# Optimization experiments

Measured on AMD Instinct MI355X. Metric: run time of the kernel, lower is better.

Reference implementation:

```python
import jax, jax.numpy as jnp
import numpy as np

D_MODEL = 512
N_HEADS = 8
D_HEAD = D_MODEL // N_HEADS
B, S = 4, 2048
NEG_INF = -1e9


def rel_shift(x):
    # x: [B,H,Q,K] -> Transformer-XL relative shift
    b, h, q, k = x.shape
    x = jnp.pad(x, ((0, 0), (0, 0), (0, 0), (1, 0)))  # [B,H,Q,K+1]
    x = x.reshape(b, h, k + 1, q)[:, :, 1:, :]          # drop first row
    return x.reshape(b, h, q, k)


def setup_inputs() -> dict:
    key = jax.random.key(0)
    ks = jax.random.split(key, 9)
    sc = 1.0 / np.sqrt(D_MODEL)
    return {
        "x": jax.random.normal(ks[0], (B, S, D_MODEL), jnp.float32),
        "pos_emb": jax.random.normal(ks[1], (S, D_MODEL), jnp.float32),
        "Wq": jax.random.normal(ks[2], (D_MODEL, D_MODEL), jnp.float32) * sc,
        "Wk": jax.random.normal(ks[3], (D_MODEL, D_MODEL), jnp.float32) * sc,
        "Wv": jax.random.normal(ks[4], (D_MODEL, D_MODEL), jnp.float32) * sc,
        "Wr": jax.random.normal(ks[5], (D_MODEL, D_MODEL), jnp.float32) * sc,
        "Wo": jax.random.normal(ks[6], (D_MODEL, D_MODEL), jnp.float32) * sc,
        "u_bias": jax.random.normal(ks[7], (N_HEADS, D_HEAD), jnp.float32) * 0.02,
        "v_bias": jax.random.normal(ks[8], (N_HEADS, D_HEAD), jnp.float32) * 0.02,
    }


def reference(x, pos_emb, Wq, Wk, Wv, Wr, Wo, u_bias, v_bias):
    b, s, _ = x.shape
    # projections -> [B,S,H,Dh]; relative pos -> [S,H,Dh]
    q = (x @ Wq).reshape(b, s, N_HEADS, D_HEAD)
    k = (x @ Wk).reshape(b, s, N_HEADS, D_HEAD)
    v = (x @ Wv).reshape(b, s, N_HEADS, D_HEAD)
    r = (pos_emb @ Wr).reshape(s, N_HEADS, D_HEAD)

    # content term (AC) and position term (BD, with rel shift)
    ac = jnp.einsum("bihd,bjhd->bhij", q + u_bias, k)
    bd = rel_shift(jnp.einsum("bihd,jhd->bhij", q + v_bias, r))

    scores = (ac + bd) / np.sqrt(D_HEAD)
    causal = jnp.tril(jnp.ones((s, s), bool))
    scores = jnp.where(causal, scores, NEG_INF)
    attn = jax.nn.softmax(scores, axis=-1)  # [B,H,S,S]

    out = jnp.einsum("bhij,bjhd->bihd", attn, v).reshape(b, s, D_MODEL)
    return out @ Wo
```

## Files before the change

### kernel.cpp

```cpp
#include <hip/hip_runtime.h>
#include <math.h>

#define SS 2048
#define BB 4
#define NHD 8
#define BH (BB * NHD)

typedef float f32x4 __attribute__((ext_vector_type(4)));
typedef __bf16 bf16x8 __attribute__((ext_vector_type(8)));

__device__ __forceinline__ short f2bf(float x) {
  unsigned u = __float_as_uint(x);
  unsigned r = (u + 0x7fffu + ((u >> 16) & 1u)) >> 16;
  return (short)r;
}

__device__ __forceinline__ void gld16(const void* g, void* l) {
  __builtin_amdgcn_global_load_lds(
      (const __attribute__((address_space(1))) unsigned int*)g,
      (__attribute__((address_space(3))) unsigned int*)l, 16, 0, 0);
}

__global__ void cast_all(const float* __restrict__ x, const float* __restrict__ pos,
                         short* __restrict__ xb, short* __restrict__ pb, int nx4) {
  int i = blockIdx.x * blockDim.x + threadIdx.x;
  const float4* src;
  short4* dst;
  if (i < nx4) {
    src = (const float4*)x + i;
    dst = (short4*)xb + i;
  } else {
    src = (const float4*)pos + (i - nx4);
    dst = (short4*)pb + (i - nx4);
  }
  float4 v = *src;
  *dst = make_short4(f2bf(v.x), f2bf(v.y), f2bf(v.z), f2bf(v.w));
}

__global__ __launch_bounds__(256) void castT_w(
    const float* __restrict__ W0, const float* __restrict__ W1,
    const float* __restrict__ W2, const float* __restrict__ W3,
    const float* __restrict__ W4, short* __restrict__ T0, short* __restrict__ T1,
    short* __restrict__ T2, short* __restrict__ T3, short* __restrict__ T4) {
  __shared__ float t[64][65];
  const float* W;
  short* T;
  switch (blockIdx.z) {
    case 0: W = W0; T = T0; break;
    case 1: W = W1; T = T1; break;
    case 2: W = W2; T = T2; break;
    case 3: W = W3; T = T3; break;
    default: W = W4; T = T4; break;
  }
  const int k0 = blockIdx.x * 64, n0 = blockIdx.y * 64;
  const int tid = threadIdx.x;
#pragma unroll
  for (int rep = 0; rep < 4; rep++) {
    int idx = rep * 256 + tid;
    int r = idx >> 4, c4 = (idx & 15) << 2;
    float4 v = *(const float4*)&W[(size_t)(k0 + r) * 512 + n0 + c4];
    t[r][c4] = v.x; t[r][c4 + 1] = v.y; t[r][c4 + 2] = v.z; t[r][c4 + 3] = v.w;
  }
  __syncthreads();
#pragma unroll
  for (int rep = 0; rep < 4; rep++) {
    int idx = rep * 256 + tid;
    int n = idx >> 4, k4 = (idx & 15) << 2;
    short4 s = make_short4(f2bf(t[k4][n]), f2bf(t[k4 + 1][n]),
                           f2bf(t[k4 + 2][n]), f2bf(t[k4 + 3][n]));
    *(short4*)&T[(size_t)(n0 + n) * 512 + k0 + k4] = s;
  }
}

__global__ __launch_bounds__(256) void conv_vt(const short* __restrict__ Vh,
                                               short* __restrict__ Vt) {
  __shared__ short t[64][72];
  const int s0 = blockIdx.x * 64, bh = blockIdx.y, tid = threadIdx.x;
#pragma unroll
  for (int rep = 0; rep < 4; rep++) {
    int idx = rep * 256 + tid;
    int r = idx >> 4, c4 = (idx & 15) << 2;
    *(short4*)&t[r][c4] = *(const short4*)&Vh[((size_t)bh * SS + s0 + r) * 64 + c4];
  }
  __syncthreads();
#pragma unroll
  for (int rep = 0; rep < 4; rep++) {
    int idx = rep * 256 + tid;
    int d = idx >> 4, s4 = (idx & 15) << 2;
    short4 o = make_short4(t[s4][d], t[s4 + 1][d], t[s4 + 2][d], t[s4 + 3][d]);
    *(short4*)&Vt[((size_t)bh * 64 + d) * SS + s0 + s4] = o;
  }
}

__device__ __forceinline__ void gemm_core(const short* __restrict__ A,
                                          const short* __restrict__ Bt,
                                          short* lds, int m0, int n0,
                                          f32x4 (&acc)[4][2]) {
  const int tid = threadIdx.x;
  const int lane = tid & 63;
  const int w = tid >> 6;
  const int wr = w >> 2, wc = w & 3;
  const int g = lane >> 4, li = lane & 15;

  auto stage = [&](int buf, int k0) {
#pragma unroll
    for (int i = 0; i < 2; i++) {
      int p = (i * 512 + tid) * 16;
      int qq = p ^ ((p >> 3) & 0x70);
      int row = qq >> 7, col = (qq & 127) >> 1;
      gld16(A + (size_t)(m0 + row) * 512 + k0 + col,
            (char*)(lds + (size_t)buf * 2 * 8192) + p);
      gld16(Bt + (size_t)(n0 + row) * 512 + k0 + col,
            (char*)(lds + ((size_t)buf * 2 + 1) * 8192) + p);
    }
  };

  stage(0, 0);
  __syncthreads();
  int buf = 0;
  for (int t = 0; t < 8; t++) {
    if (t < 7) stage(buf ^ 1, (t + 1) * 64);
    const char* As = (const char*)(lds + (size_t)buf * 2 * 8192);
    const char* Bs = (const char*)(lds + ((size_t)buf * 2 + 1) * 8192);
    bf16x8 af[4][2], bfr[2][2];
#pragma unroll
    for (int ks = 0; ks < 2; ks++) {
      const int cb = g * 16 + ks * 64;
#pragma unroll
      for (int mi = 0; mi < 4; mi++) {
        int row = wr * 64 + mi * 16 + li;
        af[mi][ks] = *(const bf16x8*)(As + row * 128 + (cb ^ ((row & 7) << 4)));
      }
#pragma unroll
      for (int ni = 0; ni < 2; ni++) {
        int row = wc * 32 + ni * 16 + li;
        bfr[ni][ks] = *(const bf16x8*)(Bs + row * 128 + (cb ^ ((row & 7) << 4)));
      }
    }
#pragma unroll
    for (int ks = 0; ks < 2; ks++)
#pragma unroll
      for (int mi = 0; mi < 4; mi++)
#pragma unroll
        for (int ni = 0; ni < 2; ni++)
          acc[mi][ni] = __builtin_amdgcn_mfma_f32_16x16x32_bf16(
              af[mi][ks], bfr[ni][ks], acc[mi][ni], 0, 0, 0);
    __syncthreads();
    buf ^= 1;
  }
}

__global__ __launch_bounds__(512) void proj_gemm(
    const short* __restrict__ A, const short* __restrict__ WtQ,
    const short* __restrict__ WtK, const short* __restrict__ WtV,
    short* __restrict__ Qu, short* __restrict__ Qv, short* __restrict__ Kb,
    short* __restrict__ Vh, const float* __restrict__ ub,
    const float* __restrict__ vb) {
  __shared__ short lds[2][2][128 * 64];
  const int z = blockIdx.z;
  const short* Bt = (z == 0) ? WtQ : (z == 1) ? WtK : WtV;
  const int m0 = blockIdx.x * 128, n0 = blockIdx.y * 128;
  f32x4 acc[4][2] = {};
  gemm_core(A, Bt, &lds[0][0][0], m0, n0, acc);

  const int tid = threadIdx.x;
  const int lane = tid & 63;
  const int w = tid >> 6;
  const int wr = w >> 2, wc = w & 3;
  const int g = lane >> 4, li = lane & 15;
#pragma unroll
  for (int mi = 0; mi < 4; mi++)
#pragma unroll
    for (int ni = 0; ni < 2; ni++) {
      const int n_g = n0 + wc * 32 + ni * 16 + li;
      const int m_b = m0 + wr * 64 + mi * 16 + g * 4;
      const int h = n_g >> 6, d = n_g & 63;
      if (z == 0) {
        const float b0 = ub[n_g], b1 = vb[n_g];
#pragma unroll
        for (int r = 0; r < 4; r++) {
          int m_g = m_b + r;
          size_t ad = ((size_t)((m_g >> 11) * NHD + h) * SS + (m_g & 2047)) * 64 + d;
          Qu[ad] = f2bf(acc[mi][ni][r] + b0);
          Qv[ad] = f2bf(acc[mi][ni][r] + b1);
        }
      } else {
        short* o = (z == 1) ? Kb : Vh;
#pragma unroll
        for (int r = 0; r < 4; r++) {
          int m_g = m_b + r;
          size_t ad = ((size_t)((m_g >> 11) * NHD + h) * SS + (m_g & 2047)) * 64 + d;
          o[ad] = f2bf(acc[mi][ni][r]);
        }
      }
    }
}

template <int EPI>
__global__ __launch_bounds__(512) void mfma_gemm(
    const short* __restrict__ A, const short* __restrict__ Bt,
    short* __restrict__ o0, float* __restrict__ of) {
  __shared__ short lds[2][2][128 * 64];
  const int m0 = blockIdx.x * 128, n0 = blockIdx.y * 128;
  f32x4 acc[4][2] = {};
  gemm_core(A, Bt, &lds[0][0][0], m0, n0, acc);

  const int tid = threadIdx.x;
  const int lane = tid & 63;
  const int w = tid >> 6;
  const int wr = w >> 2, wc = w & 3;
  const int g = lane >> 4, li = lane & 15;
#pragma unroll
  for (int mi = 0; mi < 4; mi++)
#pragma unroll
    for (int ni = 0; ni < 2; ni++) {
      const int n_g = n0 + wc * 32 + ni * 16 + li;
      const int m_b = m0 + wr * 64 + mi * 16 + g * 4;
      if (EPI == 0) {
#pragma unroll
        for (int r = 0; r < 4; r++)
          of[(size_t)(m_b + r) * 512 + n_g] = acc[mi][ni][r];
      } else {
        const int h = n_g >> 6, d = n_g & 63;
#pragma unroll
        for (int r = 0; r < 4; r++) {
          int m_g = m_b + r;
          size_t ad = ((size_t)((m_g >> 11) * NHD + h) * SS + (m_g & 2047)) * 64 + d;
          o0[ad] = f2bf(acc[mi][ni][r]);
        }
      }
    }
}

#define SC2 0.18033688f

__global__ __launch_bounds__(512, 3) void flash_mfma_kernel(
    const short* __restrict__ Qu_, const short* __restrict__ Qv_,
    const short* __restrict__ Kb_, const short* __restrict__ Vt_,
    const short* __restrict__ Rb_, short* __restrict__ AOb) {
  __shared__ __align__(16) unsigned QRl2[8][40 * 25];
  __shared__ __align__(16) short Pl[8][16 * 72];

  const int bx = blockIdx.x;
  const int bh = blockIdx.y;
  const int h = bh & 7;
  const int tid = threadIdx.x;
  const int w = tid >> 6;
  const int wq = w & 3;
  const int qi = (w < 4) ? (31 - bx) : bx;
  const int i0 = qi * 64;
  const int lane = tid & 63;
  const int q = lane & 15;
  const int g = lane >> 4;
  const int dsl = g * 8;

  unsigned* qrw = QRl2[w];
  short* pw = Pl[w];

  const size_t qoff = ((size_t)bh * SS + (i0 + wq * 16 + q)) * 64;
  bf16x8 quF[2], qvF[2];
  quF[0] = *(const bf16x8*)(Qu_ + qoff + dsl);
  quF[1] = *(const bf16x8*)(Qu_ + qoff + dsl + 32);
  qvF[0] = *(const bf16x8*)(Qv_ + qoff + dsl);
  qvF[1] = *(const bf16x8*)(Qv_ + qoff + dsl + 32);

  const int i_my = i0 + wq * 16 + q;

  float m = -1e30f, l = 0.f;
  f32x4 o[4] = {};

  for (int j0 = 0; j0 <= i0; j0 += 64) {
    bf16x8 vf[4][2];
    const size_t vtb = ((size_t)bh * 64) * SS + j0;
#pragma unroll
    for (int ds = 0; ds < 4; ds++)
#pragma unroll
      for (int c = 0; c < 2; c++)
        vf[ds][c] = *(const bf16x8*)(Vt_ + vtb + (size_t)(ds * 16 + q) * SS + dsl + 32 * c);

    f32x4 accS[4] = {};
    f32x4 accR[5] = {};
    const size_t kbase = ((size_t)bh * SS + j0) * 64;
    const int rb0 = SS - 16 + j0 - i0 - 16 * wq;
    const size_t rbase = (size_t)h * SS * 64;
    __builtin_amdgcn_s_setprio(1);
#pragma unroll
    for (int c = 0; c < 2; c++) {
      const int dof = dsl + 32 * c;
#pragma unroll
      for (int ks = 0; ks < 4; ks++) {
        bf16x8 kf = *(const bf16x8*)(Kb_ + kbase + (size_t)(ks * 16 + q) * 64 + dof);
        accS[ks] = __builtin_amdgcn_mfma_f32_16x16x32_bf16(kf, quF[c], accS[ks], 0, 0, 0);
      }
#pragma unroll
      for (int st = 0; st < 5; st++) {
        int rrow = rb0 + st * 16 + q;
        rrow = rrow < SS ? rrow : SS - 1;
        bf16x8 rf = *(const bf16x8*)(Rb_ + rbase + (size_t)rrow * 64 + dof);
        accR[st] = __builtin_amdgcn_mfma_f32_16x16x32_bf16(rf, qvF[c], accR[st], 0, 0, 0);
      }
    }
    __builtin_amdgcn_s_setprio(0);

#pragma unroll
    for (int st = 0; st < 5; st++) {
      unsigned w01 = (unsigned)(unsigned short)f2bf(accR[st][0]) |
                     ((unsigned)(unsigned short)f2bf(accR[st][1]) << 16);
      unsigned w23 = (unsigned)(unsigned short)f2bf(accR[st][2]) |
                     ((unsigned)(unsigned short)f2bf(accR[st][3]) << 16);
      int row = st * 8 + g * 2;
      qrw[row * 25 + q] = w01;
      qrw[(row + 1) * 25 + q] = w23;
    }

    float sreg[4][4];
#pragma unroll
    for (int ks = 0; ks < 4; ks++)
#pragma unroll
      for (int r = 0; r < 4; r++) {
        int krow = ks * 16 + g * 4 + r;
        int t = krow + 15 - q;
        unsigned wv = qrw[(t >> 1) * 25 + q];
        unsigned bits = (t & 1) ? (wv & 0xffff0000u) : (wv << 16);
        float qr = __uint_as_float(bits);
        float sc = (accS[ks][r] + qr) * SC2;
        sreg[ks][r] = (j0 + krow <= i_my) ? sc : -1e30f;
      }

    float b0 = fmaxf(fmaxf(sreg[0][0], sreg[0][1]), fmaxf(sreg[0][2], sreg[0][3]));
    float b1 = fmaxf(fmaxf(sreg[1][0], sreg[1][1]), fmaxf(sreg[1][2], sreg[1][3]));
    float b2 = fmaxf(fmaxf(sreg[2][0], sreg[2][1]), fmaxf(sreg[2][2], sreg[2][3]));
    float b3 = fmaxf(fmaxf(sreg[3][0], sreg[3][1]), fmaxf(sreg[3][2], sreg[3][3]));
    float bmax = fmaxf(fmaxf(b0, b1), fmaxf(b2, b3));
    bmax = fmaxf(bmax, __shfl_xor(bmax, 16, 64));
    bmax = fmaxf(bmax, __shfl_xor(bmax, 32, 64));
    float mnew = fmaxf(m, bmax);
    float scale = __builtin_amdgcn_exp2f(m - mnew);
    float ps[4];
    short4 pk[4];
#pragma unroll
    for (int ks = 0; ks < 4; ks++) {
      float p0 = __builtin_amdgcn_exp2f(sreg[ks][0] - mnew);
      float p1 = __builtin_amdgcn_exp2f(sreg[ks][1] - mnew);
      float p2 = __builtin_amdgcn_exp2f(sreg[ks][2] - mnew);
      float p3 = __builtin_amdgcn_exp2f(sreg[ks][3] - mnew);
      ps[ks] = (p0 + p1) + (p2 + p3);
      pk[ks] = make_short4(f2bf(p0), f2bf(p1), f2bf(p2), f2bf(p3));
    }
    float psum = (ps[0] + ps[1]) + (ps[2] + ps[3]);
    psum += __shfl_xor(psum, 16, 64);
    psum += __shfl_xor(psum, 32, 64);
    l = l * scale + psum;
    m = mnew;

#pragma unroll
    for (int ks = 0; ks < 4; ks++)
      *(short4*)(pw + q * 72 + ks * 16 + g * 4) = pk[ks];

#pragma unroll
    for (int r = 0; r < 4; r++) {
      float sc_r = __shfl(scale, g * 4 + r, 64);
      o[0][r] *= sc_r; o[1][r] *= sc_r; o[2][r] *= sc_r; o[3][r] *= sc_r;
    }

    bf16x8 pf[2];
    pf[0] = *(const bf16x8*)(pw + q * 72 + dsl);
    pf[1] = *(const bf16x8*)(pw + q * 72 + dsl + 32);
    __builtin_amdgcn_s_setprio(1);
#pragma unroll
    for (int ds = 0; ds < 4; ds++)
#pragma unroll
      for (int c = 0; c < 2; c++)
        o[ds] = __builtin_amdgcn_mfma_f32_16x16x32_bf16(pf[c], vf[ds][c], o[ds], 0, 0, 0);
    __builtin_amdgcn_s_setprio(0);
  }

  const int b = bh >> 3;
  float linv = 1.f / l;
#pragma unroll
  for (int r = 0; r < 4; r++) {
    float li2 = __shfl(linv, g * 4 + r, 64);
    int irow = i0 + wq * 16 + g * 4 + r;
    short* op = AOb + ((size_t)(b * SS + irow)) * 512 + h * 64 + q;
#pragma unroll
    for (int ds = 0; ds < 4; ds++) op[ds * 16] = f2bf(o[ds][r] * li2);
  }
}

extern "C" void kernel_launch(void* const* d_in, const int* in_sizes, int n_in,
                              void* d_out, int out_size, void* d_ws,
                              size_t ws_size, hipStream_t stream) {
  const float* x   = (const float*)d_in[0];
  const float* pos = (const float*)d_in[1];
  const float* Wq  = (const float*)d_in[2];
  const float* Wk  = (const float*)d_in[3];
  const float* Wv  = (const float*)d_in[4];
  const float* Wr  = (const float*)d_in[5];
  const float* Wo  = (const float*)d_in[6];
  const float* ub  = (const float*)d_in[7];
  const float* vb  = (const float*)d_in[8];
  float* out = (float*)d_out;

  const size_t BS = (size_t)BB * SS;
  const size_t NX = BS * 512;
  const size_t NR = (size_t)SS * 512;
  const size_t NW = 512 * 512;

  short* xb  = (short*)d_ws;
  short* pb  = xb + NX;
  short* WtQ = pb + NR;
  short* WtK = WtQ + NW;
  short* WtV = WtK + NW;
  short* WtR = WtV + NW;
  short* WtO = WtR + NW;
  short* Qu  = WtO + NW;
  short* Qv  = Qu + NX;
  short* Kb  = Qv + NX;
  short* Vh  = Kb + NX;
  short* Vt  = Vh + NX;
  short* Rb  = Vt + NX;
  short* AOb = Rb + NR;

  cast_all<<<dim3((NX + NR) / 4 / 256), 256, 0, stream>>>(x, pos, xb, pb, (int)(NX / 4));
  castT_w<<<dim3(8, 8, 5), 256, 0, stream>>>(Wq, Wk, Wv, Wr, Wo,
                                             WtQ, WtK, WtV, WtR, WtO);

  proj_gemm<<<dim3(64, 4, 3), 512, 0, stream>>>(xb, WtQ, WtK, WtV,
                                                Qu, Qv, Kb, Vh, ub, vb);
  mfma_gemm<2><<<dim3(16, 4), 512, 0, stream>>>(pb, WtR, Rb, nullptr);
  conv_vt<<<dim3(SS / 64, BH), 256, 0, stream>>>(Vh, Vt);

  flash_mfma_kernel<<<dim3(16, BH), 512, 0, stream>>>(Qu, Qv, Kb, Vt, Rb, AOb);

  mfma_gemm<0><<<dim3(64, 4), 512, 0, stream>>>(AOb, WtO, nullptr, out);
}
```

Measured before the change: 364.0 us.

## Split attention KV range across two blocks and merge partials in combine kernel

The flash-attention kernel moves from paired causal query tiles in 512-thread blocks to 256-thread blocks over a flat grid. Each block processes half of one query tile's key chunks and writes the partial max, sum and unnormalized bf16 output to workspace. A new combine kernel merges the two halves with log-sum-exp rescaling and writes the normalized attention output. This targets better load balance and occupancy, at the cost of an extra launch, extra global traffic, and an added bf16 rounding of the partial outputs. The setprio hints are also removed.

```diff
diff --git a/kernel.cpp b/kernel.cpp
--- a/kernel.cpp
+++ b/kernel.cpp
@@ -8,11 +8,16 @@
 
 typedef float f32x4 __attribute__((ext_vector_type(4)));
 typedef __bf16 bf16x8 __attribute__((ext_vector_type(8)));
+typedef short short8v __attribute__((ext_vector_type(8)));
 
 __device__ __forceinline__ short f2bf(float x) {
   unsigned u = __float_as_uint(x);
   unsigned r = (u + 0x7fffu + ((u >> 16) & 1u)) >> 16;
   return (short)r;
+}
+
+__device__ __forceinline__ float bf2f(short v) {
+  return __uint_as_float(((unsigned)(unsigned short)v) << 16);
 }
 
 __device__ __forceinline__ void gld16(const void* g, void* l) {
@@ -234,28 +239,29 @@
 
 #define SC2 0.18033688f
 
-__global__ __launch_bounds__(512, 3) void flash_mfma_kernel(
+__global__ __launch_bounds__(256, 8) void flash_mfma_kernel(
     const short* __restrict__ Qu_, const short* __restrict__ Qv_,
     const short* __restrict__ Kb_, const short* __restrict__ Vt_,
-    const short* __restrict__ Rb_, short* __restrict__ AOb) {
-  __shared__ __align__(16) unsigned QRl2[8][40 * 25];
-  __shared__ __align__(16) short Pl[8][16 * 72];
-
-  const int bx = blockIdx.x;
-  const int bh = blockIdx.y;
+    const short* __restrict__ Rb_, float* __restrict__ Mp,
+    float* __restrict__ Lp, short* __restrict__ Opb) {
+  __shared__ __align__(16) unsigned QRl[4][40 * 17];
+  __shared__ __align__(16) short Pl[4][16 * 72];
+
+  const int id = blockIdx.x;
+  const int z = id & 1;
+  const int bh = (id >> 1) & 31;
+  const int qi = 31 - (id >> 6);
+  const int i0 = qi * 64;
   const int h = bh & 7;
   const int tid = threadIdx.x;
-  const int w = tid >> 6;
-  const int wq = w & 3;
-  const int qi = (w < 4) ? (31 - bx) : bx;
-  const int i0 = qi * 64;
+  const int wq = tid >> 6;
   const int lane = tid & 63;
   const int q = lane & 15;
   const int g = lane >> 4;
   const int dsl = g * 8;
 
-  unsigned* qrw = QRl2[w];
-  short* pw = Pl[w];
+  unsigned* qrw = QRl[wq];
+  short* pw = Pl[wq];
 
   const size_t qoff = ((size_t)bh * SS + (i0 + wq * 16 + q)) * 64;
   bf16x8 quF[2], qvF[2];
@@ -266,10 +272,16 @@
 
   const int i_my = i0 + wq * 16 + q;
 
+  const int nch = qi + 1;
+  const int half = (nch + 1) >> 1;
+  const int cc0 = z ? half : 0;
+  const int cc1 = z ? nch : half;
+
   float m = -1e30f, l = 0.f;
   f32x4 o[4] = {};
 
-  for (int j0 = 0; j0 <= i0; j0 += 64) {
+  for (int cc = cc0; cc < cc1; cc++) {
+    const int j0 = cc * 64;
     bf16x8 vf[4][2];
     const size_t vtb = ((size_t)bh * 64) * SS + j0;
 #pragma unroll
@@ -283,7 +295,6 @@
     const size_t kbase = ((size_t)bh * SS + j0) * 64;
     const int rb0 = SS - 16 + j0 - i0 - 16 * wq;
     const size_t rbase = (size_t)h * SS * 64;
-    __builtin_amdgcn_s_setprio(1);
 #pragma unroll
     for (int c = 0; c < 2; c++) {
       const int dof = dsl + 32 * c;
@@ -300,7 +311,6 @@
         accR[st] = __builtin_amdgcn_mfma_f32_16x16x32_bf16(rf, qvF[c], accR[st], 0, 0, 0);
       }
     }
-    __builtin_amdgcn_s_setprio(0);
 
 #pragma unroll
     for (int st = 0; st < 5; st++) {
@@ -309,8 +319,8 @@
       unsigned w23 = (unsigned)(unsigned short)f2bf(accR[st][2]) |
                      ((unsigned)(unsigned short)f2bf(accR[st][3]) << 16);
       int row = st * 8 + g * 2;
-      qrw[row * 25 + q] = w01;
-      qrw[(row + 1) * 25 + q] = w23;
+      qrw[row * 17 + q] = w01;
+      qrw[(row + 1) * 17 + q] = w23;
     }
 
     float sreg[4][4];
@@ -320,7 +330,7 @@
       for (int r = 0; r < 4; r++) {
         int krow = ks * 16 + g * 4 + r;
         int t = krow + 15 - q;
-        unsigned wv = qrw[(t >> 1) * 25 + q];
+        unsigned wv = qrw[(t >> 1) * 17 + q];
         unsigned bits = (t & 1) ? (wv & 0xffff0000u) : (wv << 16);
         float qr = __uint_as_float(bits);
         float sc = (accS[ks][r] + qr) * SC2;
@@ -366,25 +376,45 @@
     bf16x8 pf[2];
     pf[0] = *(const bf16x8*)(pw + q * 72 + dsl);
     pf[1] = *(const bf16x8*)(pw + q * 72 + dsl + 32);
-    __builtin_amdgcn_s_setprio(1);
 #pragma unroll
     for (int ds = 0; ds < 4; ds++)
 #pragma unroll
       for (int c = 0; c < 2; c++)
         o[ds] = __builtin_amdgcn_mfma_f32_16x16x32_bf16(pf[c], vf[ds][c], o[ds], 0, 0, 0);
-    __builtin_amdgcn_s_setprio(0);
-  }
-
-  const int b = bh >> 3;
-  float linv = 1.f / l;
-#pragma unroll
-  for (int r = 0; r < 4; r++) {
-    float li2 = __shfl(linv, g * 4 + r, 64);
-    int irow = i0 + wq * 16 + g * 4 + r;
-    short* op = AOb + ((size_t)(b * SS + irow)) * 512 + h * 64 + q;
-#pragma unroll
-    for (int ds = 0; ds < 4; ds++) op[ds * 16] = f2bf(o[ds][r] * li2);
-  }
+  }
+
+  const int prow = (z * 32 + bh) * SS + i0 + wq * 16;
+  if (g == 0) {
+    Mp[prow + q] = m;
+    Lp[prow + q] = l;
+  }
+#pragma unroll
+  for (int r = 0; r < 4; r++)
+#pragma unroll
+    for (int ds = 0; ds < 4; ds++)
+      Opb[(size_t)(prow + g * 4 + r) * 64 + ds * 16 + q] = f2bf(o[ds][r]);
+}
+
+__global__ __launch_bounds__(256) void combine_kernel(
+    const float* __restrict__ Mp, const float* __restrict__ Lp,
+    const short* __restrict__ Opb, short* __restrict__ AOb) {
+  const int t = blockIdx.x * 256 + threadIdx.x;
+  const int row = t >> 3;
+  const int d0 = (t & 7) * 8;
+  const float m0 = Mp[row], m1 = Mp[65536 + row];
+  const float l0 = Lp[row], l1 = Lp[65536 + row];
+  const float M = fmaxf(m0, m1);
+  const float s0 = __builtin_amdgcn_exp2f(m0 - M);
+  const float s1 = __builtin_amdgcn_exp2f(m1 - M);
+  const float inv = 1.f / (l0 * s0 + l1 * s1);
+  short8v a = *(const short8v*)(Opb + (size_t)row * 64 + d0);
+  short8v b = *(const short8v*)(Opb + (size_t)(65536 + row) * 64 + d0);
+  short8v out;
+#pragma unroll
+  for (int e = 0; e < 8; e++)
+    out[e] = f2bf((bf2f(a[e]) * s0 + bf2f(b[e]) * s1) * inv);
+  const int bh = row >> 11, i = row & 2047;
+  *(short8v*)(AOb + ((size_t)((bh >> 3) * SS + i)) * 512 + (bh & 7) * 64 + d0) = out;
 }
 
 extern "C" void kernel_launch(void* const* d_in, const int* in_sizes, int n_in,
@@ -420,6 +450,9 @@
   short* Vt  = Vh + NX;
   short* Rb  = Vt + NX;
   short* AOb = Rb + NR;
+  float* Mp  = (float*)(AOb + NX);
+  float* Lp  = Mp + 2 * 65536;
+  short* Opb = (short*)(Lp + 2 * 65536);
 
   cast_all<<<dim3((NX + NR) / 4 / 256), 256, 0, stream>>>(x, pos, xb, pb, (int)(NX / 4));
   castT_w<<<dim3(8, 8, 5), 256, 0, stream>>>(Wq, Wk, Wv, Wr, Wo,
@@ -430,7 +463,9 @@
   mfma_gemm<2><<<dim3(16, 4), 512, 0, stream>>>(pb, WtR, Rb, nullptr);
   conv_vt<<<dim3(SS / 64, BH), 256, 0, stream>>>(Vh, Vt);
 
-  flash_mfma_kernel<<<dim3(16, BH), 512, 0, stream>>>(Qu, Qv, Kb, Vt, Rb, AOb);
+  flash_mfma_kernel<<<dim3(2048), 256, 0, stream>>>(Qu, Qv, Kb, Vt, Rb,
+                                                    Mp, Lp, Opb);
+  combine_kernel<<<dim3(2048), 256, 0, stream>>>(Mp, Lp, Opb, AOb);
 
   mfma_gemm<0><<<dim3(64, 4), 512, 0, stream>>>(AOb, WtO, nullptr, out);
 }
```

After: 487.4 us. 1.34x slower.
